# Performance work log

Measured on AMD Instinct MI355X. Metric: run time of the kernel, lower is better.

The kernel has to match this reference:

```python
import jax, jax.numpy as jnp
import numpy as np

B, C, D, Hh, W = 2, 320, 4, 16, 16
N = D * Hh * W          # 1024 nodes
NH = 8                  # num_heads
DH = C // NH            # 40
L = 2                   # num_layers
A, EPD = 16, 64         # da_prior tokens, encode_prior_dim
EDGE_SCALE = 32 ** -0.5 # GraphEdgeFeature dim_head=32
SCALE = DH ** -0.5
EPS = 1e-5


def _ln(x, g, b):
    m = x.mean(-1, keepdims=True)
    v = ((x - m) ** 2).mean(-1, keepdims=True)
    return (x - m) * jax.lax.rsqrt(v + EPS) * g + b


def setup_inputs() -> dict:
    key = jax.random.key(0)
    ks = jax.random.split(key, 16)
    std = 0.02 / np.sqrt(L)
    inp = {
        'x': jax.random.normal(ks[0], (B, C, D, Hh, W), jnp.float32),
        'da_prior': jax.random.normal(ks[1], (B, A, EPD), jnp.float32),
        # GraphEdgeFeature.to_qk (no bias), init std 0.02/sqrt(24)
        'qk_w': jax.random.normal(ks[2], (2 * C, C), jnp.float32) * (0.02 / np.sqrt(24)),
        # fc_prior
        'fcp_w': jax.random.normal(ks[3], (C, EPD), jnp.float32) * 0.02,
        'fcp_b': jnp.zeros((C,), jnp.float32),
        # per-layer (stacked over L)
        'ln1_g': jnp.ones((L, C), jnp.float32),
        'ln1_b': jnp.zeros((L, C), jnp.float32),
        'gln_g': jnp.ones((L, C), jnp.float32),
        'gln_b': jnp.zeros((L, C), jnp.float32),
        'qkv_w': jax.random.normal(ks[4], (L, 3 * C, C), jnp.float32) * std,
        'qkv_b': jnp.zeros((L, 3 * C), jnp.float32),
        'proj_w': jax.random.normal(ks[5], (L, C, C), jnp.float32) * std,
        'proj_b': jnp.zeros((L, C), jnp.float32),
        # expand Conv2d(1, NH, 1): weight [NH], bias [NH]
        'exp_w': jax.random.normal(ks[6], (L, NH), jnp.float32),
        'exp_b': jnp.zeros((L, NH), jnp.float32),
        # reduce Conv2d(NH, 1, 1): weight [NH], bias scalar
        'red_w': jax.random.normal(ks[7], (L, NH), jnp.float32) / np.sqrt(NH),
        'red_b': jnp.zeros((L,), jnp.float32),
    }
    return inp


def _forward(x, da_prior, qk_w, fcp_w, fcp_b, ln1_g, ln1_b, gln_g, gln_b,
             qkv_w, qkv_b, proj_w, proj_b, exp_w, exp_b, red_w, red_b):
    node = x.reshape(B, C, N)                       # [B,C,N]
    # ---- GraphEdgeFeature: full-dim QK attention over nodes ----
    xt = node.transpose(0, 2, 1)                    # [B,N,C]
    qk = xt @ qk_w.T                                # [B,N,2C]
    q_e, k_e = jnp.split(qk, 2, axis=-1)
    edge = jax.nn.softmax(jnp.einsum('bqc,bkc->bqk', q_e, k_e) * EDGE_SCALE, axis=-1)  # [B,N,N]
    # ---- fc_prior ----
    da = da_prior @ fcp_w.T + fcp_b                 # [B,A,C]
    s = da.sum(axis=1)                              # [B,C] (sum over 'a' in einsum bnc,bca->bnc)
    for l in range(L):
        # block norm1 over channel dim
        nt = _ln(node.transpose(0, 2, 1), ln1_g[l], ln1_b[l])   # [B,N,C]
        # torch.einsum('bnn,bnc->bnc') takes the DIAGONAL of edge
        diag = jnp.diagonal(edge, axis1=1, axis2=2)             # [B,N]
        node2 = diag[:, :, None] * nt * s[:, None, :] + nt      # [B,N,C]
        y = _ln(node2, gln_g[l], gln_b[l])
        qkv = (y @ qkv_w[l].T + qkv_b[l]).reshape(B, N, 3, NH, DH)
        qkv = qkv.transpose(2, 0, 3, 1, 4)                      # [3,B,H,N,DH]
        q, k, v = qkv[0], qkv[1], qkv[2]
        attn = jnp.einsum('bhnd,bhmd->bhnm', q, k) * SCALE
        attn = attn + edge[:, None] * exp_w[l][None, :, None, None] + exp_b[l][None, :, None, None]
        a = jax.nn.softmax(attn, axis=-1)                       # [B,H,N,N]
        node_out = jnp.einsum('bhnm,bhmd->bhnd', a, v).transpose(0, 2, 1, 3).reshape(B, N, C)
        edge_new = jnp.einsum('bhnm,h->bnm', a + attn, red_w[l]) + red_b[l]  # [B,N,N]
        ws = jax.nn.softmax(edge_new, axis=-1)
        wsum = (ws * edge_new).sum(-1)                          # [B,N]
        node_out = node_out + wsum[:, :, None]                  # fc=Identity, broadcast
        node_out = node_out @ proj_w[l].T + proj_b[l]
        node = node_out.transpose(0, 2, 1)                      # [B,C,N]
        edge = edge + edge_new
    return node.reshape(B, C, D, Hh, W)


def reference(x, da_prior, qk_w, fcp_w, fcp_b, ln1_g, ln1_b, gln_g, gln_b,
              qkv_w, qkv_b, proj_w, proj_b, exp_w, exp_b, red_w, red_b):
    return _forward(x, da_prior, qk_w, fcp_w, fcp_b, ln1_g, ln1_b, gln_g, gln_b,
                    qkv_w, qkv_b, proj_w, proj_b, exp_w, exp_b, red_w, red_b)
```

## Files before the change

kernel.cpp:

```cpp
#include <hip/hip_runtime.h>
#include <math.h>

#define EDGE_SCALE 0.17677669529663687f
#define ATT_SCALE  0.15811388300841897f
#define LN_EPS 1e-5f

typedef __attribute__((ext_vector_type(8))) short bf8;
typedef __attribute__((ext_vector_type(4))) float f32x4;

__device__ __forceinline__ f32x4 mfma16(bf8 a, bf8 b, f32x4 c) {
  return __builtin_amdgcn_mfma_f32_16x16x32_bf16(a, b, c, 0, 0, 0);
}
__device__ __forceinline__ unsigned short f2bf(float f) {
  union { float f; unsigned u; } v; v.f = f;
  unsigned r = v.u + 0x7FFF + ((v.u >> 16) & 1);
  return (unsigned short)(r >> 16);
}
__device__ __forceinline__ float bf2f(unsigned short h) {
  union { unsigned u; float f; } v; v.u = ((unsigned)h) << 16;
  return v.f;
}
__device__ __forceinline__ float wave_max(float v) {
  #pragma unroll
  for (int o = 32; o > 0; o >>= 1) v = fmaxf(v, __shfl_xor(v, o));
  return v;
}
__device__ __forceinline__ float wave_sum(float v) {
  #pragma unroll
  for (int o = 32; o > 0; o >>= 1) v += __shfl_xor(v, o);
  return v;
}

__global__ __launch_bounds__(256) void k_trans(const float* __restrict__ x,
    float* __restrict__ node, unsigned short* __restrict__ nodebf) {
  __shared__ float tile[32][33];
  const int b = blockIdx.z;
  const int n0 = blockIdx.x * 32, c0 = blockIdx.y * 32;
  const int tx = threadIdx.x & 31, ty = threadIdx.x >> 5;
  #pragma unroll
  for (int k = 0; k < 4; ++k) {
    int c = c0 + ty + 8 * k;
    tile[ty + 8 * k][tx] = x[((size_t)b * 320 + c) * 1024 + n0 + tx];
  }
  __syncthreads();
  #pragma unroll
  for (int k = 0; k < 4; ++k) {
    int n = n0 + ty + 8 * k;
    float v = tile[tx][ty + 8 * k];
    size_t idx = ((size_t)b * 1024 + n) * 320 + c0 + tx;
    node[idx] = v;
    nodebf[idx] = f2bf(v);
  }
}

__global__ __launch_bounds__(320) void k_svec(const float* __restrict__ da,
    const float* __restrict__ fw, const float* __restrict__ fb, float* __restrict__ sv) {
  __shared__ float ds[64];
  const int b = blockIdx.x, t = threadIdx.x;
  if (t < 64) {
    float a = 0.f;
    #pragma unroll
    for (int i = 0; i < 16; ++i) a += da[b * 1024 + i * 64 + t];
    ds[t] = a;
  }
  __syncthreads();
  if (t < 320) {
    float acc = 16.f * fb[t];
    #pragma unroll
    for (int e = 0; e < 64; ++e) acc = fmaf(ds[e], fw[t * 64 + e], acc);
    sv[b * 320 + t] = acc;
  }
}

__global__ void k_wcvt(const float* __restrict__ a, int na,
                       const float* __restrict__ b, int nb,
                       const float* __restrict__ c, int nc,
                       unsigned short* __restrict__ out,
                       uint4* __restrict__ zbuf, int zn4) {
  int tot = na + nb + nc;
  for (int i = blockIdx.x * blockDim.x + threadIdx.x; i < tot; i += gridDim.x * blockDim.x) {
    float v = (i < na) ? a[i] : ((i < na + nb) ? b[i - na] : c[i - na - nb]);
    out[i] = f2bf(v);
  }
  const uint4 z = {0u, 0u, 0u, 0u};
  for (int i = blockIdx.x * blockDim.x + threadIdx.x; i < zn4; i += gridDim.x * blockDim.x)
    zbuf[i] = z;
}

__global__ __launch_bounds__(256, 4) void k_mgemm(
    const unsigned short* __restrict__ A, const unsigned short* __restrict__ W,
    const float* __restrict__ bias, void* p0, void* p1, void* p2, int mode) {
  __shared__ float smem[64 * 65];
  const int t = threadIdx.x, w = t >> 6, lane = t & 63;
  const int q16 = lane >> 4, l16 = lane & 15;
  const int rt = blockIdx.x * 64, jt = blockIdx.y * 64;
  f32x4 acc[4];
  #pragma unroll
  for (int i = 0; i < 4; ++i)
    #pragma unroll
    for (int j = 0; j < 4; ++j) acc[i][j] = 0.f;
  const unsigned short* ap = A + (size_t)(rt + 16 * w + l16) * 320 + q16 * 8;
  const unsigned short* wp = W + (size_t)(jt + l16) * 320 + q16 * 8;
  for (int kc = 0; kc < 10; ++kc) {
    bf8 af = *(const bf8*)(ap + kc * 32);
    #pragma unroll
    for (int ct = 0; ct < 4; ++ct) {
      bf8 bf = *(const bf8*)(wp + (size_t)ct * 16 * 320 + kc * 32);
      acc[ct] = mfma16(af, bf, acc[ct]);
    }
  }
  if (mode == 0 || mode == 1) {
    #pragma unroll
    for (int ct = 0; ct < 4; ++ct) {
      int col = jt + ct * 16 + l16;
      float bv = bias ? bias[col] : 0.f;
      #pragma unroll
      for (int r = 0; r < 4; ++r) {
        int row = rt + 16 * w + q16 * 4 + r;
        float v = acc[ct][r] + bv;
        if (mode == 0) {
          ((float*)p0)[(size_t)row * 320 + col] = v;
        } else {
          if (col < 320) ((unsigned short*)p0)[(size_t)row * 320 + col] = f2bf(v);
          else           ((unsigned short*)p1)[(size_t)row * 320 + col - 320] = f2bf(v);
        }
      }
    }
  } else if (mode == 2) {
    const int part = jt / 320;
    if (part < 2) {
      unsigned short* dst = (unsigned short*)(part == 0 ? p0 : p1);
      #pragma unroll
      for (int ct = 0; ct < 4; ++ct) {
        int col = jt + ct * 16 + l16;
        float bv = bias[col];
        int rem = col - part * 320;
        int h = rem / 40, d = rem % 40;
        #pragma unroll
        for (int r = 0; r < 4; ++r) {
          int row = rt + 16 * w + q16 * 4 + r;
          int b = row >> 10, n = row & 1023;
          dst[(((size_t)b * 8 + h) * 1024 + n) * 64 + d] = f2bf(acc[ct][r] + bv);
        }
      }
    } else {
      unsigned short* vt_t = (unsigned short*)smem;
      #pragma unroll
      for (int ct = 0; ct < 4; ++ct) {
        int col = jt + ct * 16 + l16;
        float bv = bias[col];
        #pragma unroll
        for (int r = 0; r < 4; ++r)
          vt_t[(ct * 16 + l16) * 72 + 16 * w + q16 * 4 + r] = f2bf(acc[ct][r] + bv);
      }
      __syncthreads();
      const int cl = t >> 2, seg = t & 3;
      int rem = (jt - 640) + cl;
      int h = rem / 40, d = rem % 40;
      int b = rt >> 10, n = (rt & 1023) + seg * 16;
      const float4* lp = (const float4*)&vt_t[cl * 72 + seg * 16];
      float4 a0 = lp[0], a1 = lp[1];
      float4* gp = (float4*)((unsigned short*)p2 +
                             (((size_t)b * 8 + h) * 48 + d) * 1024 + n);
      gp[0] = a0; gp[1] = a1;
    }
  } else {
    #pragma unroll
    for (int ct = 0; ct < 4; ++ct) {
      int col = jt + ct * 16 + l16;
      float bv = bias[col];
      #pragma unroll
      for (int r = 0; r < 4; ++r)
        smem[(16 * w + q16 * 4 + r) * 65 + ct * 16 + l16] = acc[ct][r] + bv;
    }
    __syncthreads();
    const int cl = t >> 2, seg = t & 3;
    int b = rt >> 10, n = (rt & 1023) + seg * 16;
    float* orow = (float*)p0 + ((size_t)b * 320 + jt + cl) * 1024 + n;
    #pragma unroll
    for (int i2 = 0; i2 < 4; ++i2) {
      float4 vv;
      vv.x = smem[(seg * 16 + i2 * 4 + 0) * 65 + cl];
      vv.y = smem[(seg * 16 + i2 * 4 + 1) * 65 + cl];
      vv.z = smem[(seg * 16 + i2 * 4 + 2) * 65 + cl];
      vv.w = smem[(seg * 16 + i2 * 4 + 3) * 65 + cl];
      ((float4*)orow)[i2] = vv;
    }
  }
}

__global__ __launch_bounds__(512, 2) void k_edge3(
    const unsigned short* __restrict__ qe, const unsigned short* __restrict__ ke,
    float* __restrict__ edge) {
  __shared__ float zred[8][16];
  const int t = threadIdx.x, w = t >> 6, lane = t & 63;
  const int q16 = lane >> 4, l16 = lane & 15;
  const int n0 = blockIdx.x * 16, b = blockIdx.y;
  const unsigned short* qp = qe + ((size_t)(b * 1024 + n0 + l16)) * 320 + q16 * 8;
  bf8 af[10];
  #pragma unroll
  for (int kc = 0; kc < 10; ++kc) af[kc] = *(const bf8*)(qp + kc * 32);
  f32x4 acc[8];
  #pragma unroll
  for (int i = 0; i < 8; ++i)
    #pragma unroll
    for (int j = 0; j < 4; ++j) acc[i][j] = 0.f;
  const unsigned short* kp = ke + ((size_t)(b * 1024 + w * 128 + l16)) * 320 + q16 * 8;
  #pragma unroll
  for (int mt = 0; mt < 8; ++mt) {
    const unsigned short* kpt = kp + (size_t)mt * 16 * 320;
    #pragma unroll
    for (int kc = 0; kc < 10; ++kc) {
      bf8 bf = *(const bf8*)(kpt + kc * 32);
      acc[mt] = mfma16(af[kc], bf, acc[mt]);
    }
  }
  float zp[4] = {0.f, 0.f, 0.f, 0.f};
  #pragma unroll
  for (int mt = 0; mt < 8; ++mt)
    #pragma unroll
    for (int r = 0; r < 4; ++r) {
      float e = __expf(acc[mt][r] * EDGE_SCALE);
      acc[mt][r] = e;
      zp[r] += e;
    }
  #pragma unroll
  for (int r = 0; r < 4; ++r)
    #pragma unroll
    for (int o = 1; o <= 8; o <<= 1) zp[r] += __shfl_xor(zp[r], o);
  if (l16 == 0) {
    #pragma unroll
    for (int r = 0; r < 4; ++r) zred[w][q16 * 4 + r] = zp[r];
  }
  __syncthreads();
  float inv[4];
  #pragma unroll
  for (int r = 0; r < 4; ++r) {
    float s = 0.f;
    #pragma unroll
    for (int ww = 0; ww < 8; ++ww) s += zred[ww][q16 * 4 + r];
    inv[r] = 1.f / s;
  }
  #pragma unroll
  for (int r = 0; r < 4; ++r) {
    float* ep = edge + ((size_t)(b * 1024 + n0 + q16 * 4 + r)) * 1024 + w * 128 + l16;
    #pragma unroll
    for (int mt = 0; mt < 8; ++mt) ep[mt * 16] = acc[mt][r] * inv[r];
  }
}

__global__ __launch_bounds__(256) void k_ln(const float* __restrict__ node,
    const float* __restrict__ edge, const float* __restrict__ sv,
    const float* __restrict__ g1, const float* __restrict__ b1,
    const float* __restrict__ g2, const float* __restrict__ b2,
    unsigned short* __restrict__ y) {
  const int w = threadIdx.x >> 6, lane = threadIdx.x & 63;
  const int row = blockIdx.x * 4 + w;
  const int b = row >> 10, n = row & 1023;
  const float* xr = node + (size_t)row * 320;
  float x[5];
  #pragma unroll
  for (int i = 0; i < 5; ++i) x[i] = xr[lane + 64 * i];
  float s = x[0] + x[1] + x[2] + x[3] + x[4];
  float mean = wave_sum(s) * (1.f / 320.f);
  float v = 0.f;
  #pragma unroll
  for (int i = 0; i < 5; ++i) { float d = x[i] - mean; v += d * d; }
  float rstd = rsqrtf(wave_sum(v) * (1.f / 320.f) + LN_EPS);
  float diag = edge[(size_t)row * 1024 + n];
  float n2[5];
  #pragma unroll
  for (int i = 0; i < 5; ++i) {
    int c = lane + 64 * i;
    float nt = (x[i] - mean) * rstd * g1[c] + b1[c];
    n2[i] = diag * nt * sv[b * 320 + c] + nt;
  }
  s = n2[0] + n2[1] + n2[2] + n2[3] + n2[4];
  float mean2 = wave_sum(s) * (1.f / 320.f);
  v = 0.f;
  #pragma unroll
  for (int i = 0; i < 5; ++i) { float d = n2[i] - mean2; v += d * d; }
  float rstd2 = rsqrtf(wave_sum(v) * (1.f / 320.f) + LN_EPS);
  unsigned short* yr = y + (size_t)row * 320;
  #pragma unroll
  for (int i = 0; i < 5; ++i) {
    int c = lane + 64 * i;
    yr[c] = f2bf((n2[i] - mean2) * rstd2 * g2[c] + b2[c]);
  }
}

__global__ __launch_bounds__(256, 2) void k_score2(
    const unsigned short* __restrict__ qbf, const unsigned short* __restrict__ kbf,
    const unsigned short* __restrict__ vtb, const float* __restrict__ edge,
    unsigned short* __restrict__ th, float* __restrict__ att,
    const float* __restrict__ ew, const float* __restrict__ eb,
    const float* __restrict__ rw) {
  __shared__ unsigned short a_lds[4][4][16][20];
  __shared__ float ored[2][4][3][16][17];
  __shared__ float zred[2][4][16];
  const int t = threadIdx.x, w = t >> 6, lane = t & 63;
  const int q16 = lane >> 4, l16 = lane & 15;
  const int n0 = blockIdx.x * 16, hp = blockIdx.y, b = blockIdx.z;
  float t_reg[16][4];
  #pragma unroll
  for (int tt = 0; tt < 16; ++tt)
    #pragma unroll
    for (int r = 0; r < 4; ++r) t_reg[tt][r] = 0.f;
  f32x4 oacc[2][3];
  #pragma unroll
  for (int hh = 0; hh < 2; ++hh)
    #pragma unroll
    for (int i = 0; i < 3; ++i)
      #pragma unroll
      for (int j = 0; j < 4; ++j) oacc[hh][i][j] = 0.f;
  const float* ep = edge + ((size_t)(b * 1024 + n0 + q16 * 4)) * 1024 + w * 256 + l16;
  #pragma unroll 1
  for (int hh = 0; hh < 2; ++hh) {
    const int h = hp * 2 + hh;
    const size_t bh = (size_t)b * 8 + h;
    const float ewh = ew[h], ebh = eb[h], rwh = rw[h];
    const unsigned short* qp = qbf + (bh * 1024 + n0 + l16) * 64 + q16 * 8;
    bf8 af0 = *(const bf8*)(qp);
    bf8 af1 = *(const bf8*)(qp + 32);
    f32x4 acc[16];
    #pragma unroll
    for (int i = 0; i < 16; ++i)
      #pragma unroll
      for (int j = 0; j < 4; ++j) acc[i][j] = 0.f;
    const unsigned short* kp = kbf + (bh * 1024 + (size_t)w * 256 + l16) * 64 + q16 * 8;
    #pragma unroll
    for (int tt = 0; tt < 16; ++tt) {
      const unsigned short* kpt = kp + (size_t)tt * 16 * 64;
      bf8 b0 = *(const bf8*)(kpt);
      bf8 b1 = *(const bf8*)(kpt + 32);
      acc[tt] = mfma16(af0, b0, acc[tt]);
      acc[tt] = mfma16(af1, b1, acc[tt]);
    }
    float zp[4] = {0.f, 0.f, 0.f, 0.f};
    #pragma unroll
    for (int tt = 0; tt < 16; ++tt)
      #pragma unroll
      for (int r = 0; r < 4; ++r) {
        float ev = ep[(size_t)r * 1024 + tt * 16];
        float s = fmaf(acc[tt][r], ATT_SCALE, fmaf(ev, ewh, ebh));
        acc[tt][r] = s;
        zp[r] += __expf(s);
      }
    #pragma unroll
    for (int r = 0; r < 4; ++r)
      #pragma unroll
      for (int o = 1; o <= 8; o <<= 1) zp[r] += __shfl_xor(zp[r], o);
    if (l16 == 0) {
      #pragma unroll
      for (int r = 0; r < 4; ++r) zred[hh][w][q16 * 4 + r] = zp[r];
    }
    __syncthreads();
    float invZ[4];
    #pragma unroll
    for (int r = 0; r < 4; ++r)
      invZ[r] = 1.f / (zred[hh][0][q16 * 4 + r] + zred[hh][1][q16 * 4 + r] +
                       zred[hh][2][q16 * 4 + r] + zred[hh][3][q16 * 4 + r]);
    #pragma unroll
    for (int g = 0; g < 4; ++g) {
      #pragma unroll
      for (int ti = 0; ti < 4; ++ti) {
        int tt = g * 4 + ti;
        #pragma unroll
        for (int r = 0; r < 4; ++r) {
          float s = acc[tt][r];
          float e = __expf(s);
          a_lds[w][ti][q16 * 4 + r][l16] = f2bf(e * invZ[r]);
          t_reg[tt][r] = fmaf(rwh, fmaf(e, invZ[r], s), t_reg[tt][r]);
        }
      }
      #pragma unroll
      for (int kk = 0; kk < 2; ++kk) {
        const unsigned short* ap2 = &a_lds[w][kk * 2 + (q16 >> 1)][l16][(q16 & 1) * 8];
        short4 lo = *(const short4*)(ap2);
        short4 hi = *(const short4*)(ap2 + 4);
        bf8 afv = {lo.x, lo.y, lo.z, lo.w, hi.x, hi.y, hi.z, hi.w};
        int kc = w * 8 + g * 2 + kk;
        const unsigned short* vp = vtb + (bh * 48 + l16) * 1024 + (size_t)kc * 32 + q16 * 8;
        #pragma unroll
        for (int nt = 0; nt < 3; ++nt) {
          bf8 bfv = *(const bf8*)(vp + (size_t)nt * 16 * 1024);
          oacc[hh][nt] = mfma16(afv, bfv, oacc[hh][nt]);
        }
      }
    }
  }
  {
    unsigned short* tp = th + (((size_t)(b * 4 + hp)) * 1024 + n0 + q16 * 4) * 1024
                         + w * 256 + l16;
    #pragma unroll
    for (int tt = 0; tt < 16; ++tt)
      #pragma unroll
      for (int r = 0; r < 4; ++r)
        tp[(size_t)r * 1024 + tt * 16] = f2bf(t_reg[tt][r]);
  }
  #pragma unroll
  for (int hh = 0; hh < 2; ++hh)
    #pragma unroll
    for (int nt = 0; nt < 3; ++nt)
      #pragma unroll
      for (int r = 0; r < 4; ++r) ored[hh][w][nt][q16 * 4 + r][l16] = oacc[hh][nt][r];
  __syncthreads();
  #pragma unroll
  for (int hh = 0; hh < 2; ++hh) {
    #pragma unroll
    for (int k = 0; k < 3; ++k) {
      int o = k * 256 + t;
      int nt = o >> 8, row = (o >> 4) & 15, col = o & 15;
      int dim = nt * 16 + col;
      float sum = ored[hh][0][nt][row][col] + ored[hh][1][nt][row][col] +
                  ored[hh][2][nt][row][col] + ored[hh][3][nt][row][col];
      if (dim < 40)
        att[((size_t)b * 1024 + n0 + row) * 320 + (hp * 2 + hh) * 40 + dim] = sum;
    }
  }
}

__global__ __launch_bounds__(256) void k_wsum(
    const unsigned short* __restrict__ th, float* __restrict__ edge,
    const float* __restrict__ att, unsigned short* __restrict__ attbf,
    const float* __restrict__ rb) {
  const int w = threadIdx.x >> 6, lane = threadIdx.x & 63;
  const int row = blockIdx.x * 4 + w;
  const int b = row >> 10, n = row & 1023;
  const float rbv = rb[0];
  float tv[16];
  #pragma unroll
  for (int i = 0; i < 16; ++i) tv[i] = rbv;
  #pragma unroll 1
  for (int hp = 0; hp < 4; ++hp) {
    const unsigned short* tph = th + (((size_t)b * 4 + hp) * 1024 + n) * 1024 + lane * 4;
    #pragma unroll
    for (int seg = 0; seg < 4; ++seg) {
      ushort4 u = *(const ushort4*)(tph + seg * 256);
      tv[seg * 4 + 0] += bf2f(u.x);
      tv[seg * 4 + 1] += bf2f(u.y);
      tv[seg * 4 + 2] += bf2f(u.z);
      tv[seg * 4 + 3] += bf2f(u.w);
    }
  }
  float4* erp = (float4*)(edge + ((size_t)b * 1024 + n) * 1024) + lane;
  #pragma unroll
  for (int seg = 0; seg < 4; ++seg) {
    float4 e = erp[seg * 64];
    e.x += tv[seg * 4 + 0]; e.y += tv[seg * 4 + 1];
    e.z += tv[seg * 4 + 2]; e.w += tv[seg * 4 + 3];
    erp[seg * 64] = e;
  }
  float mx = -3.4e38f;
  #pragma unroll
  for (int i = 0; i < 16; ++i) mx = fmaxf(mx, tv[i]);
  mx = wave_max(mx);
  float s = 0.f, num = 0.f;
  #pragma unroll
  for (int i = 0; i < 16; ++i) {
    float e = __expf(tv[i] - mx);
    s += e; num += e * tv[i];
  }
  s = wave_sum(s); num = wave_sum(num);
  const float wsum = num / s;
  const float* ar = att + (size_t)row * 320;
  unsigned short* ao = attbf + (size_t)row * 320;
  #pragma unroll
  for (int i = 0; i < 5; ++i) {
    int c = lane + 64 * i;
    ao[c] = f2bf(ar[c] + wsum);
  }
}

extern "C" void kernel_launch(void* const* d_in, const int* in_sizes, int n_in,
                              void* d_out, int out_size, void* d_ws, size_t ws_size,
                              hipStream_t stream) {
  const float* x      = (const float*)d_in[0];
  const float* da     = (const float*)d_in[1];
  const float* qk_w   = (const float*)d_in[2];
  const float* fcp_w  = (const float*)d_in[3];
  const float* fcp_b  = (const float*)d_in[4];
  const float* ln1_g  = (const float*)d_in[5];
  const float* ln1_b  = (const float*)d_in[6];
  const float* gln_g  = (const float*)d_in[7];
  const float* gln_b  = (const float*)d_in[8];
  const float* qkv_w  = (const float*)d_in[9];
  const float* qkv_b  = (const float*)d_in[10];
  const float* proj_w = (const float*)d_in[11];
  const float* proj_b = (const float*)d_in[12];
  const float* exp_w  = (const float*)d_in[13];
  const float* exp_b  = (const float*)d_in[14];
  const float* red_w  = (const float*)d_in[15];
  const float* red_b  = (const float*)d_in[16];
  float* ws = (float*)d_ws;
  float* node  = ws + 0;
  unsigned short* ybf   = (unsigned short*)(ws + 655360);
  float* attb  = ws + 983040;
  unsigned short* attbf = (unsigned short*)(ws + 1638400);
  float* edge  = ws + 1966080;
  float* svec  = ws + 4063232;
  unsigned short* nodebf = (unsigned short*)(ws + 4063872);
  unsigned short* qe   = (unsigned short*)(ws + 4391552);
  unsigned short* ke   = (unsigned short*)(ws + 4719232);
  unsigned short* qbf  = (unsigned short*)(ws + 5046912);
  unsigned short* kbf  = (unsigned short*)(ws + 5571200);
  unsigned short* vtb  = (unsigned short*)(ws + 6095488);
  unsigned short* wbf  = (unsigned short*)(ws + 6488704);
  unsigned short* th   = (unsigned short*)(ws + 7000704);
  float* out = (float*)d_out;
  unsigned short* qk_wb   = wbf;
  unsigned short* qkv_wb  = wbf + 204800;
  unsigned short* proj_wb = wbf + 819200;

  hipLaunchKernelGGL(k_trans, dim3(32, 10, 2), dim3(256), 0, stream, x, node, nodebf);
  hipLaunchKernelGGL(k_svec, dim3(2), dim3(320), 0, stream, da, fcp_w, fcp_b, svec);
  hipLaunchKernelGGL(k_wcvt, dim3(512), dim3(256), 0, stream,
                     qk_w, 204800, qkv_w, 614400, proj_w, 204800, wbf,
                     (uint4*)qbf, 262144);
  hipLaunchKernelGGL(k_mgemm, dim3(32, 10), dim3(256), 0, stream,
                     nodebf, qk_wb, (const float*)nullptr, qe, ke, (void*)nullptr, 1);
  hipLaunchKernelGGL(k_edge3, dim3(64, 2), dim3(512), 0, stream, qe, ke, edge);
  for (int l = 0; l < 2; ++l) {
    hipLaunchKernelGGL(k_ln, dim3(512), dim3(256), 0, stream, node, edge, svec,
                       ln1_g + l * 320, ln1_b + l * 320, gln_g + l * 320, gln_b + l * 320, ybf);
    hipLaunchKernelGGL(k_mgemm, dim3(32, 15), dim3(256), 0, stream,
                       ybf, qkv_wb + (size_t)l * 307200, qkv_b + l * 960, qbf, kbf, vtb, 2);
    hipLaunchKernelGGL(k_score2, dim3(64, 4, 2), dim3(256), 0, stream,
                       qbf, kbf, vtb, edge, th, attb,
                       exp_w + l * 8, exp_b + l * 8, red_w + l * 8);
    hipLaunchKernelGGL(k_wsum, dim3(512), dim3(256), 0, stream,
                       th, edge, attb, attbf, red_b + l);
    if (l == 0)
      hipLaunchKernelGGL(k_mgemm, dim3(32, 5), dim3(256), 0, stream,
                         attbf, proj_wb, proj_b, node, (void*)nullptr, (void*)nullptr, 0);
    else
      hipLaunchKernelGGL(k_mgemm, dim3(32, 5), dim3(256), 0, stream,
                         attbf, proj_wb + 102400, proj_b + 320, out,
                         (void*)nullptr, (void*)nullptr, 3);
  }
}
```

Before: 340.8 us.

## Split score kernel to one head per block and drop register accumulators

The score kernel now processes a single head per block instead of a pair of heads. This removes the 64-float per-thread t_reg accumulator, which allows a launch bound of 4 blocks per CU and doubles the grid. Each block writes its head's scaled (a+attn) term straight to the th buffer, and the wsum kernel now sums over 8 per-head slices instead of 4 pair slices. The cost is twice the th traffic and twice the fp32 edge reads. The th allocation must also hold 8 slices instead of 4.

Result: faster. 294.1 us (-13.7%).

```diff
diff --git a/kernel.cpp b/kernel.cpp
--- a/kernel.cpp
+++ b/kernel.cpp
@@ -289,134 +289,111 @@
   }
 }
 
-__global__ __launch_bounds__(256, 2) void k_score2(
+__global__ __launch_bounds__(256, 4) void k_score3(
     const unsigned short* __restrict__ qbf, const unsigned short* __restrict__ kbf,
     const unsigned short* __restrict__ vtb, const float* __restrict__ edge,
     unsigned short* __restrict__ th, float* __restrict__ att,
     const float* __restrict__ ew, const float* __restrict__ eb,
     const float* __restrict__ rw) {
   __shared__ unsigned short a_lds[4][4][16][20];
-  __shared__ float ored[2][4][3][16][17];
-  __shared__ float zred[2][4][16];
+  __shared__ float ored[4][3][16][17];
+  __shared__ float zred[4][16];
   const int t = threadIdx.x, w = t >> 6, lane = t & 63;
   const int q16 = lane >> 4, l16 = lane & 15;
-  const int n0 = blockIdx.x * 16, hp = blockIdx.y, b = blockIdx.z;
-  float t_reg[16][4];
+  const int n0 = blockIdx.x * 16, h = blockIdx.y, b = blockIdx.z;
+  const size_t bh = (size_t)b * 8 + h;
+  const unsigned short* qp = qbf + (bh * 1024 + n0 + l16) * 64 + q16 * 8;
+  bf8 af0 = *(const bf8*)(qp);
+  bf8 af1 = *(const bf8*)(qp + 32);
+  f32x4 acc[16];
+  #pragma unroll
+  for (int i = 0; i < 16; ++i)
+    #pragma unroll
+    for (int j = 0; j < 4; ++j) acc[i][j] = 0.f;
+  const unsigned short* kp = kbf + (bh * 1024 + (size_t)w * 256 + l16) * 64 + q16 * 8;
+  #pragma unroll
+  for (int tt = 0; tt < 16; ++tt) {
+    const unsigned short* kpt = kp + (size_t)tt * 16 * 64;
+    bf8 b0 = *(const bf8*)(kpt);
+    bf8 b1 = *(const bf8*)(kpt + 32);
+    acc[tt] = mfma16(af0, b0, acc[tt]);
+    acc[tt] = mfma16(af1, b1, acc[tt]);
+  }
+  const float ewh = ew[h], ebh = eb[h], rwh = rw[h];
+  const float* ep = edge + ((size_t)b * 1024 + n0 + q16 * 4) * 1024 + w * 256 + l16;
+  float zp[4] = {0.f, 0.f, 0.f, 0.f};
   #pragma unroll
   for (int tt = 0; tt < 16; ++tt)
     #pragma unroll
-    for (int r = 0; r < 4; ++r) t_reg[tt][r] = 0.f;
-  f32x4 oacc[2][3];
-  #pragma unroll
-  for (int hh = 0; hh < 2; ++hh)
-    #pragma unroll
-    for (int i = 0; i < 3; ++i)
-      #pragma unroll
-      for (int j = 0; j < 4; ++j) oacc[hh][i][j] = 0.f;
-  const float* ep = edge + ((size_t)(b * 1024 + n0 + q16 * 4)) * 1024 + w * 256 + l16;
-  #pragma unroll 1
-  for (int hh = 0; hh < 2; ++hh) {
-    const int h = hp * 2 + hh;
-    const size_t bh = (size_t)b * 8 + h;
-    const float ewh = ew[h], ebh = eb[h], rwh = rw[h];
-    const unsigned short* qp = qbf + (bh * 1024 + n0 + l16) * 64 + q16 * 8;
-    bf8 af0 = *(const bf8*)(qp);
-    bf8 af1 = *(const bf8*)(qp + 32);
-    f32x4 acc[16];
-    #pragma unroll
-    for (int i = 0; i < 16; ++i)
-      #pragma unroll
-      for (int j = 0; j < 4; ++j) acc[i][j] = 0.f;
-    const unsigned short* kp = kbf + (bh * 1024 + (size_t)w * 256 + l16) * 64 + q16 * 8;
-    #pragma unroll
-    for (int tt = 0; tt < 16; ++tt) {
-      const unsigned short* kpt = kp + (size_t)tt * 16 * 64;
-      bf8 b0 = *(const bf8*)(kpt);
-      bf8 b1 = *(const bf8*)(kpt + 32);
-      acc[tt] = mfma16(af0, b0, acc[tt]);
-      acc[tt] = mfma16(af1, b1, acc[tt]);
-    }
-    float zp[4] = {0.f, 0.f, 0.f, 0.f};
-    #pragma unroll
-    for (int tt = 0; tt < 16; ++tt)
+    for (int r = 0; r < 4; ++r) {
+      float ev = ep[(size_t)r * 1024 + tt * 16];
+      float s = fmaf(acc[tt][r], ATT_SCALE, fmaf(ev, ewh, ebh));
+      acc[tt][r] = s;
+      zp[r] += __expf(s);
+    }
+  #pragma unroll
+  for (int r = 0; r < 4; ++r)
+    #pragma unroll
+    for (int o = 1; o <= 8; o <<= 1) zp[r] += __shfl_xor(zp[r], o);
+  if (l16 == 0) {
+    #pragma unroll
+    for (int r = 0; r < 4; ++r) zred[w][q16 * 4 + r] = zp[r];
+  }
+  __syncthreads();
+  float invZ[4];
+  #pragma unroll
+  for (int r = 0; r < 4; ++r)
+    invZ[r] = 1.f / (zred[0][q16 * 4 + r] + zred[1][q16 * 4 + r] +
+                     zred[2][q16 * 4 + r] + zred[3][q16 * 4 + r]);
+  f32x4 oacc[3];
+  #pragma unroll
+  for (int i = 0; i < 3; ++i)
+    #pragma unroll
+    for (int j = 0; j < 4; ++j) oacc[i][j] = 0.f;
+  unsigned short* tp = th + (bh * 1024 + n0 + q16 * 4) * 1024 + w * 256 + l16;
+  #pragma unroll
+  for (int g = 0; g < 4; ++g) {
+    #pragma unroll
+    for (int ti = 0; ti < 4; ++ti) {
+      int tt = g * 4 + ti;
       #pragma unroll
       for (int r = 0; r < 4; ++r) {
-        float ev = ep[(size_t)r * 1024 + tt * 16];
-        float s = fmaf(acc[tt][r], ATT_SCALE, fmaf(ev, ewh, ebh));
-        acc[tt][r] = s;
-        zp[r] += __expf(s);
+        float s = acc[tt][r];
+        float e = __expf(s);
+        float a = e * invZ[r];
+        a_lds[w][ti][q16 * 4 + r][l16] = f2bf(a);
+        tp[(size_t)r * 1024 + tt * 16] = f2bf(rwh * (a + s));
       }
-    #pragma unroll
-    for (int r = 0; r < 4; ++r)
+    }
+    #pragma unroll
+    for (int kk = 0; kk < 2; ++kk) {
+      const unsigned short* ap2 = &a_lds[w][kk * 2 + (q16 >> 1)][l16][(q16 & 1) * 8];
+      short4 lo = *(const short4*)(ap2);
+      short4 hi = *(const short4*)(ap2 + 4);
+      bf8 afv = {lo.x, lo.y, lo.z, lo.w, hi.x, hi.y, hi.z, hi.w};
+      int kc = w * 8 + g * 2 + kk;
+      const unsigned short* vp = vtb + (bh * 48 + l16) * 1024 + (size_t)kc * 32 + q16 * 8;
       #pragma unroll
-      for (int o = 1; o <= 8; o <<= 1) zp[r] += __shfl_xor(zp[r], o);
-    if (l16 == 0) {
-      #pragma unroll
-      for (int r = 0; r < 4; ++r) zred[hh][w][q16 * 4 + r] = zp[r];
-    }
-    __syncthreads();
-    float invZ[4];
-    #pragma unroll
-    for (int r = 0; r < 4; ++r)
-      invZ[r] = 1.f / (zred[hh][0][q16 * 4 + r] + zred[hh][1][q16 * 4 + r] +
-                       zred[hh][2][q16 * 4 + r] + zred[hh][3][q16 * 4 + r]);
-    #pragma unroll
-    for (int g = 0; g < 4; ++g) {
-      #pragma unroll
-      for (int ti = 0; ti < 4; ++ti) {
-        int tt = g * 4 + ti;
-        #pragma unroll
-        for (int r = 0; r < 4; ++r) {
-          float s = acc[tt][r];
-          float e = __expf(s);
-          a_lds[w][ti][q16 * 4 + r][l16] = f2bf(e * invZ[r]);
-          t_reg[tt][r] = fmaf(rwh, fmaf(e, invZ[r], s), t_reg[tt][r]);
-        }
+      for (int nt = 0; nt < 3; ++nt) {
+        bf8 bfv = *(const bf8*)(vp + (size_t)nt * 16 * 1024);
+        oacc[nt] = mfma16(afv, bfv, oacc[nt]);
       }
-      #pragma unroll
-      for (int kk = 0; kk < 2; ++kk) {
-        const unsigned short* ap2 = &a_lds[w][kk * 2 + (q16 >> 1)][l16][(q16 & 1) * 8];
-        short4 lo = *(const short4*)(ap2);
-        short4 hi = *(const short4*)(ap2 + 4);
-        bf8 afv = {lo.x, lo.y, lo.z, lo.w, hi.x, hi.y, hi.z, hi.w};
-        int kc = w * 8 + g * 2 + kk;
-        const unsigned short* vp = vtb + (bh * 48 + l16) * 1024 + (size_t)kc * 32 + q16 * 8;
-        #pragma unroll
-        for (int nt = 0; nt < 3; ++nt) {
-          bf8 bfv = *(const bf8*)(vp + (size_t)nt * 16 * 1024);
-          oacc[hh][nt] = mfma16(afv, bfv, oacc[hh][nt]);
-        }
-      }
-    }
-  }
-  {
-    unsigned short* tp = th + (((size_t)(b * 4 + hp)) * 1024 + n0 + q16 * 4) * 1024
-                         + w * 256 + l16;
-    #pragma unroll
-    for (int tt = 0; tt < 16; ++tt)
-      #pragma unroll
-      for (int r = 0; r < 4; ++r)
-        tp[(size_t)r * 1024 + tt * 16] = f2bf(t_reg[tt][r]);
-  }
-  #pragma unroll
-  for (int hh = 0; hh < 2; ++hh)
-    #pragma unroll
-    for (int nt = 0; nt < 3; ++nt)
-      #pragma unroll
-      for (int r = 0; r < 4; ++r) ored[hh][w][nt][q16 * 4 + r][l16] = oacc[hh][nt][r];
+    }
+  }
+  #pragma unroll
+  for (int nt = 0; nt < 3; ++nt)
+    #pragma unroll
+    for (int r = 0; r < 4; ++r) ored[w][nt][q16 * 4 + r][l16] = oacc[nt][r];
   __syncthreads();
   #pragma unroll
-  for (int hh = 0; hh < 2; ++hh) {
-    #pragma unroll
-    for (int k = 0; k < 3; ++k) {
-      int o = k * 256 + t;
-      int nt = o >> 8, row = (o >> 4) & 15, col = o & 15;
-      int dim = nt * 16 + col;
-      float sum = ored[hh][0][nt][row][col] + ored[hh][1][nt][row][col] +
-                  ored[hh][2][nt][row][col] + ored[hh][3][nt][row][col];
-      if (dim < 40)
-        att[((size_t)b * 1024 + n0 + row) * 320 + (hp * 2 + hh) * 40 + dim] = sum;
-    }
+  for (int k = 0; k < 3; ++k) {
+    int o = k * 256 + t;
+    int nt = o >> 8, row = (o >> 4) & 15, col = o & 15;
+    int dim = nt * 16 + col;
+    float sum = ored[0][nt][row][col] + ored[1][nt][row][col] +
+                ored[2][nt][row][col] + ored[3][nt][row][col];
+    if (dim < 40)
+      att[((size_t)b * 1024 + n0 + row) * 320 + h * 40 + dim] = sum;
   }
 }
 
@@ -432,8 +409,8 @@
   #pragma unroll
   for (int i = 0; i < 16; ++i) tv[i] = rbv;
   #pragma unroll 1
-  for (int hp = 0; hp < 4; ++hp) {
-    const unsigned short* tph = th + (((size_t)b * 4 + hp) * 1024 + n) * 1024 + lane * 4;
+  for (int h = 0; h < 8; ++h) {
+    const unsigned short* tph = th + (((size_t)b * 8 + h) * 1024 + n) * 1024 + lane * 4;
     #pragma unroll
     for (int seg = 0; seg < 4; ++seg) {
       ushort4 u = *(const ushort4*)(tph + seg * 256);
@@ -525,7 +502,7 @@
                        ln1_g + l * 320, ln1_b + l * 320, gln_g + l * 320, gln_b + l * 320, ybf);
     hipLaunchKernelGGL(k_mgemm, dim3(32, 15), dim3(256), 0, stream,
                        ybf, qkv_wb + (size_t)l * 307200, qkv_b + l * 960, qbf, kbf, vtb, 2);
-    hipLaunchKernelGGL(k_score2, dim3(64, 4, 2), dim3(256), 0, stream,
+    hipLaunchKernelGGL(k_score3, dim3(64, 8, 2), dim3(256), 0, stream,
                        qbf, kbf, vtb, edge, th, attb,
                        exp_w + l * 8, exp_b + l * 8, red_w + l * 8);
     hipLaunchKernelGGL(k_wsum, dim3(512), dim3(256), 0, stream,
```
